# Performance work log

Hardware: AMD Instinct MI355X
Metric: run time of the kernel (lower is better)

The kernel has to match this reference:

```python
import jax, jax.numpy as jnp
import numpy as np
import math

# ---- static configuration (matches init_kwargs / input_specs) ----
N = 512       # nodes
CIN = 32      # input multiplicity per irrep l
C = 32        # num_channels
LMAX = 4      # input/output lmax
D = (LMAX + 1) ** 2   # 25 real-SH components
RB = 48       # res_beta (Gauss-Legendre nodes in cos(beta))
RA = 95       # res_alpha (uniform)
NB = 3        # parity branches (p1,p2) in {(1,1),(1,-1),(-1,1)}


def _assoc_legendre(lmax, x):
    """Associated Legendre P_l^m(x) with Condon-Shortley phase. [l, m, len(x)]."""
    P = np.zeros((lmax + 1, lmax + 1, len(x)))
    P[0, 0] = 1.0
    sx = np.sqrt(np.maximum(0.0, 1.0 - x * x))
    for m in range(1, lmax + 1):
        P[m, m] = -(2 * m - 1) * sx * P[m - 1, m - 1]
    for m in range(lmax):
        P[m + 1, m] = (2 * m + 1) * x * P[m, m]
    for l in range(2, lmax + 1):
        for m in range(0, l - 1):
            P[l, m] = ((2 * l - 1) * x * P[l - 1, m] - (l + m - 1) * P[l - 2, m]) / (l - m)
    return P


def _real_sh_grid(lmax, rb, ra):
    """Real orthonormal SH sampled on (beta, alpha) grid + quadrature-weighted basis.
    Returns Y [(lmax+1)^2, rb, ra] and Yw (Y * w_beta * dalpha) so that
    einsum('dba,eba->de', Y, Yw) ~= identity (exact SHT / inverse SHT pair)."""
    xq, wq = np.polynomial.legendre.leggauss(rb)   # x = cos(beta), GL quadrature
    P = _assoc_legendre(lmax, xq)
    alpha = 2.0 * np.pi * np.arange(ra) / ra
    Dd = (lmax + 1) ** 2
    Y = np.zeros((Dd, rb, ra))
    for l in range(lmax + 1):
        for m in range(0, l + 1):
            Nlm = math.sqrt((2 * l + 1) / (4 * math.pi) * math.factorial(l - m) / math.factorial(l + m))
            if m == 0:
                Y[l * l + l] = Nlm * P[l, 0][:, None] * np.ones((1, ra))
            else:
                Y[l * l + l + m] = math.sqrt(2.0) * Nlm * P[l, m][:, None] * np.cos(m * alpha)[None, :]
                Y[l * l + l - m] = math.sqrt(2.0) * Nlm * P[l, m][:, None] * np.sin(m * alpha)[None, :]
    Yw = Y * wq[None, :, None] * (2.0 * np.pi / ra)
    return Y.astype(np.float32), Yw.astype(np.float32)

_Y_NP, _YW_NP = _real_sh_grid(LMAX, RB, RA)


def setup_inputs() -> dict:
    key = jax.random.key(0)
    ks = jax.random.split(key, 6)
    s_in = 1.0 / np.sqrt(CIN)
    return {
        "x1": jax.random.normal(ks[0], (N, CIN, D), jnp.float32),
        "x2": jax.random.normal(ks[1], (N, CIN, D), jnp.float32),
        "W1": jax.random.normal(ks[2], (NB, LMAX, CIN, C), jnp.float32) * s_in,
        "W2": jax.random.normal(ks[3], (NB, LMAX, CIN, C), jnp.float32) * s_in,
        "Wout0": jax.random.normal(ks[4], (NB, C + CIN, C + CIN), jnp.float32) / np.sqrt(C + CIN),
        "WoutL": jax.random.normal(ks[5], (NB, LMAX, C, C), jnp.float32) / np.sqrt(C),
    }


def _project(x, W):
    """Equivariant Linear: per-l channel mixing CIN->C, dropping l=0 (filter drop 0e/0o).
    x [N, CIN, D], W [LMAX, CIN, C] -> [N, C, D] with l=0 slot zero."""
    parts = [jnp.zeros((x.shape[0], W.shape[-1], 1), x.dtype)]
    for l in range(1, LMAX + 1):
        xl = x[:, :, l * l:(l + 1) * (l + 1)]            # [N, CIN, 2l+1]
        parts.append(jnp.einsum('nkm,kc->ncm', xl, W[l - 1]))
    return jnp.concatenate(parts, axis=-1)


def reference(x1, x2, W1, W2, Wout0, WoutL):
    Y = jnp.asarray(_Y_NP)    # [D, RB, RA]
    Yw = jnp.asarray(_YW_NP)  # quadrature-weighted basis for the inverse transform
    n = x1.shape[0]
    outs = []
    for b in range(NB):  # three parity branches, distinct learned weights
        c1 = _project(x1, W1[b])                      # [N, C, D]
        c2 = _project(x2, W2[b])
        f1 = jnp.einsum('ncd,dba->ncba', c1, Y)        # to S2 grid [N, C, RB, RA]
        f2 = jnp.einsum('ncd,dba->ncba', c2, Y)
        cp = jnp.einsum('ncba,dba->ncd', f1 * f2, Yw)  # pointwise product + inverse SHT
        s = x1[:, :, 0] * x2[:, :, 0]                  # scalar CG tensor product [N, CIN]
        o0 = jnp.concatenate([cp[:, :, 0], s], axis=1) @ Wout0[b]   # l=0 output mix
        oL = [jnp.einsum('ncm,cd->ndm', cp[:, :, l * l:(l + 1) * (l + 1)], WoutL[b, l - 1]).reshape(n, -1)
              for l in range(1, LMAX + 1)]
        outs.append(jnp.concatenate([o0] + oL, axis=1))
    return jnp.concatenate(outs, axis=1)  # [N, 3*(C+CIN + C*(D-1))] = [512, 2496]
```

## Files before the change

kernel.cpp:

```cpp
#include <hip/hip_runtime.h>
#include <math.h>

#define DDIM 25
#define RB 48
#define RA 95
#define OUT_PER_B 832
#define OUT_STRIDE 2496
#define PI_D 3.14159265358979323846

#define SEG_I  8
#define ENT_I  64
#define ENT_CAP 2600
#define TRIP_CAP 2600

__device__ int g_ready = 0;
__device__ int g_tab[ENT_I + 2 * ENT_CAP];

__constant__ int L_OF_D[25] = {0,1,1,1,2,2,2,2,2,3,3,3,3,3,3,3,4,4,4,4,4,4,4,4,4};

__device__ __forceinline__ float bf2f(unsigned short u) {
    return __uint_as_float(((unsigned int)u) << 16);
}
__device__ __forceinline__ unsigned short f2bf(float f) {
    unsigned int x = __float_as_uint(f);
    return (unsigned short)((x + 0x7FFFu + ((x >> 16) & 1u)) >> 16);
}

__global__ __launch_bounds__(1024) void setup_kernel() {
    if (g_ready) return;

    __shared__ double xg[RB], wq[RB];
    __shared__ double Rl[DDIM * RB];
    __shared__ double cosT[RA * 5], sinT[RA * 5];
    __shared__ double AS[729];
    __shared__ double invT[64];
    __shared__ int cnt[DDIM], cnt2[DDIM];
    __shared__ int segl[DDIM + 1];
    __shared__ int tripl[TRIP_CAP];
    __shared__ int ntrip;
    const int t = threadIdx.x;
    const int BT = 1024;

    if (t == 0) ntrip = 0;
    if (t < DDIM) { cnt[t] = 0; cnt2[t] = 0; }
    if (t < 64) invT[t] = (t == 0) ? 0.0 : 1.0 / (double)t;
    __syncthreads();

    if (t < RB) {
        double x = cos(PI_D * (t + 0.75) / (RB + 0.5));
        double p0, p1, dp;
        for (int it = 0; it < 5; ++it) {
            p0 = 1.0; p1 = x;
            for (int k = 2; k <= RB; ++k) {
                double p2 = ((2.0 * k - 1.0) * x * p1 - (k - 1.0) * p0) * invT[k];
                p0 = p1; p1 = p2;
            }
            dp = RB * (x * p1 - p0) / (x * x - 1.0);
            x -= p1 / dp;
        }
        p0 = 1.0; p1 = x;
        for (int k = 2; k <= RB; ++k) {
            double p2 = ((2.0 * k - 1.0) * x * p1 - (k - 1.0) * p0) * invT[k];
            p0 = p1; p1 = p2;
        }
        dp = RB * (x * p1 - p0) / (x * x - 1.0);
        xg[t] = x;
        wq[t] = 2.0 / ((1.0 - x * x) * dp * dp);
    }
    for (int idx = t; idx < RA * 5; idx += BT) {
        int a = idx / 5, mm = idx % 5;
        double ang = 2.0 * PI_D * (double)(mm * a) / (double)RA;
        cosT[idx] = cos(ang);
        sinT[idx] = sin(ang);
    }
    __syncthreads();

    for (int idx = t; idx < DDIM * RB; idx += BT) {
        int d = idx / RB, b = idx % RB;
        int l = L_OF_D[d];
        int m = d - l * l - l;
        int am = m < 0 ? -m : m;
        double x = xg[b];
        double sx = sqrt(fmax(0.0, 1.0 - x * x));
        double pmm = 1.0;
        for (int k = 1; k <= am; ++k) pmm = -(2.0 * k - 1.0) * sx * pmm;
        double res;
        if (l == am) res = pmm;
        else {
            double pprev = pmm;
            double pcur = (2.0 * am + 1.0) * x * pmm;
            for (int ll = am + 2; ll <= l; ++ll) {
                double pnext = ((2.0 * ll - 1.0) * x * pcur - (double)(ll + am - 1) * pprev) * invT[ll - am];
                pprev = pcur; pcur = pnext;
            }
            res = pcur;
        }
        double fr = 1.0;
        for (int j = l - am + 1; j <= l + am; ++j) fr *= (double)j;
        double Nlm = sqrt((2.0 * l + 1.0) / (4.0 * PI_D) / fr);
        if (m != 0) Nlm *= sqrt(2.0);
        Rl[d * RB + b] = Nlm * res;
    }
    __syncthreads();

    for (int idx = t; idx < 729; idx += BT) {
        int m1 = idx / 81 - 4, m2 = (idx / 9) % 9 - 4, m3 = idx % 9 - 4;
        double s = 0.0;
        for (int a = 0; a < RA; ++a) {
            double t1 = (m1 == 0) ? 1.0 : (m1 > 0 ? cosT[a * 5 + m1] : sinT[a * 5 - m1]);
            double t2 = (m2 == 0) ? 1.0 : (m2 > 0 ? cosT[a * 5 + m2] : sinT[a * 5 - m2]);
            double t3 = (m3 == 0) ? 1.0 : (m3 > 0 ? cosT[a * 5 + m3] : sinT[a * 5 - m3]);
            s += t1 * t2 * t3;
        }
        AS[idx] = s * (2.0 * PI_D / (double)RA);
    }
    __syncthreads();

    for (int idx = t; idx < 24 * 24 * 25; idx += BT) {
        int d3 = idx % 25;
        int r = idx / 25;
        int dd2 = r % 24, dd1 = r / 24;
        int d1 = dd1 + 1, d2 = dd2 + 1;
        int l1 = L_OF_D[d1], l2 = L_OF_D[d2], l3 = L_OF_D[d3];
        if ((l1 + l2 + l3) & 1) continue;
        if (l3 < abs(l1 - l2) || l3 > l1 + l2) continue;
        int m1 = d1 - l1 * l1 - l1, m2 = d2 - l2 * l2 - l2, m3 = d3 - l3 * l3 - l3;
        if (fabs(AS[(m1 + 4) * 81 + (m2 + 4) * 9 + (m3 + 4)]) < 1e-6) continue;
        int pos = atomicAdd(&ntrip, 1);
        if (pos < TRIP_CAP) {
            tripl[pos] = (d3 << 16) | (dd1 << 8) | dd2;
            atomicAdd(&cnt[d3], 1);
        }
    }
    __syncthreads();
    if (t == 0) {
        segl[0] = 0;
        for (int d = 0; d < DDIM; ++d) segl[d + 1] = segl[d] + cnt[d];
        for (int d = 0; d <= DDIM; ++d) g_tab[SEG_I + d] = segl[d];
    }
    __syncthreads();

    {
        int nt = ntrip < TRIP_CAP ? ntrip : TRIP_CAP;
        uint2* ent = (uint2*)(g_tab + ENT_I);
        for (int i = t; i < nt; i += BT) {
            int pk = tripl[i];
            int d3 = pk >> 16, dd1 = (pk >> 8) & 255, dd2 = pk & 255;
            int d1 = dd1 + 1, d2 = dd2 + 1;
            int l1 = L_OF_D[d1], l2 = L_OF_D[d2], l3 = L_OF_D[d3];
            int m1 = d1 - l1 * l1 - l1, m2 = d2 - l2 * l2 - l2, m3 = d3 - l3 * l3 - l3;
            const double* r1 = &Rl[d1 * RB];
            const double* r2 = &Rl[d2 * RB];
            const double* r3 = &Rl[d3 * RB];
            double s0 = 0.0, s1 = 0.0, s2 = 0.0, s3 = 0.0;
            for (int b = 0; b < RB; b += 4) {
                s0 += wq[b + 0] * r1[b + 0] * r2[b + 0] * r3[b + 0];
                s1 += wq[b + 1] * r1[b + 1] * r2[b + 1] * r3[b + 1];
                s2 += wq[b + 2] * r1[b + 2] * r2[b + 2] * r3[b + 2];
                s3 += wq[b + 3] * r1[b + 3] * r2[b + 3] * r3[b + 3];
            }
            double g = (s0 + s1 + s2 + s3) * AS[(m1 + 4) * 81 + (m2 + 4) * 9 + (m3 + 4)];
            int pos = atomicAdd(&cnt2[d3], 1);
            int at = segl[d3] + pos;
            if (at < ENT_CAP)
                ent[at] = make_uint2((unsigned)((dd1 << 8) | dd2), __float_as_uint((float)g));
        }
    }
    __syncthreads();
    if (t == 0) g_ready = 1;
}

template <int ISF32>
__device__ __forceinline__ void stageW(const void* Wv, int b, float* wbuf, int t) {
    if (ISF32) {
        const float* w = (const float*)Wv + b * 4096;
        #pragma unroll
        for (int i = 0; i < 8; ++i) wbuf[t + 512 * i] = w[t + 512 * i];
    } else {
        const unsigned* w = (const unsigned*)Wv + b * 2048;
        #pragma unroll
        for (int i = 0; i < 4; ++i) {
            unsigned v = w[t + 512 * i];
            wbuf[2 * (t + 512 * i)]     = bf2f((unsigned short)(v & 0xFFFF));
            wbuf[2 * (t + 512 * i) + 1] = bf2f((unsigned short)(v >> 16));
        }
    }
}

__device__ __forceinline__ void mix_pair(const float* __restrict__ xs,
                                         const float* __restrict__ wbuf,
                                         float* __restrict__ cs, int t) {
    if (t >= 384) return;
    int j = t & 15;
    int dd = t >> 4;
    int d = dd + 1;
    int l = L_OF_D[d];
    const float* wv = &wbuf[(l - 1) * 1024 + 2 * j];
    const float* xv = &xs[2 * d];
    float a00 = 0.f, a01 = 0.f, a10 = 0.f, a11 = 0.f;
    #pragma unroll
    for (int k = 0; k < 32; ++k) {
        float2 w = *(const float2*)&wv[k * 32];
        float2 x = *(const float2*)&xv[k * 50];
        a00 += x.x * w.x; a01 += x.x * w.y;
        a10 += x.y * w.x; a11 += x.y * w.y;
    }
    int c0 = 2 * j, c1 = 2 * j + 1;
    cs[2 * (c0 * 25 + dd) + 0] = a00;
    cs[2 * (c0 * 25 + dd) + 1] = a10;
    cs[2 * (c1 * 25 + dd) + 0] = a01;
    cs[2 * (c1 * 25 + dd) + 1] = a11;
}

template <int ISF32>
__device__ __forceinline__ void main_body(
    const void* __restrict__ x1v, const void* __restrict__ x2v,
    const void* __restrict__ W1v, const void* __restrict__ W2v,
    const void* __restrict__ Wo0v, const void* __restrict__ WoLv,
    void* __restrict__ outv,
    float* wbuf, float* x1s, float* x2s, float* c1s, float* c2s, float* cps,
    const int t, const int np, const int b)
{
    const int s = t >> 8;
    const int tl = t & 255;
    const int n = np * 2 + s;

    if (ISF32) {
        const float* x1f = (const float*)x1v + n * 800;
        const float* x2f = (const float*)x2v + n * 800;
        for (int i = tl; i < 800; i += 256) {
            x1s[2 * i + s] = x1f[i];
            x2s[2 * i + s] = x2f[i];
        }
    } else {
        const unsigned* x1u = (const unsigned*)x1v + n * 400;
        const unsigned* x2u = (const unsigned*)x2v + n * 400;
        for (int i = tl; i < 400; i += 256) {
            unsigned v1 = x1u[i], v2 = x2u[i];
            x1s[4 * i + s]     = bf2f((unsigned short)(v1 & 0xFFFF));
            x1s[4 * i + 2 + s] = bf2f((unsigned short)(v1 >> 16));
            x2s[4 * i + s]     = bf2f((unsigned short)(v2 & 0xFFFF));
            x2s[4 * i + 2 + s] = bf2f((unsigned short)(v2 >> 16));
        }
    }
    stageW<ISF32>(W1v, b, wbuf, t);
    __syncthreads();

    mix_pair(x1s, wbuf, c1s, t);
    __syncthreads();
    stageW<ISF32>(W2v, b, wbuf, t);
    __syncthreads();
    mix_pair(x2s, wbuf, c2s, t);
    __syncthreads();

    {
        const int* seg = g_tab + SEG_I;
        const uint2* ent = (const uint2*)(g_tab + ENT_I);
        int c = t & 31;
        int gq = t >> 5;
        const float* c1p = &c1s[50 * c];
        const float* c2p = &c2s[50 * c];
        for (int d3 = gq; d3 < 25; d3 += 16) {
            int j1 = seg[d3 + 1];
            float a0 = 0.f, a1 = 0.f;
            for (int j = seg[d3]; j < j1; ++j) {
                uint2 e = ent[j];
                float gf = __uint_as_float(e.y);
                float2 u = *(const float2*)&c1p[2 * (e.x >> 8)];
                float2 v = *(const float2*)&c2p[2 * (e.x & 255)];
                a0 += gf * u.x * v.x;
                a1 += gf * u.y * v.y;
            }
            *(float2*)&cps[2 * (c * 25 + d3)] = make_float2(a0, a1);
        }
    }
    stageW<ISF32>(WoLv, b, wbuf, t);
    __syncthreads();

    const int obase0 = (np * 2) * OUT_STRIDE + b * OUT_PER_B;
    const int obase1 = obase0 + OUT_STRIDE;
    if (t < 384) {
        int dout = t & 31;
        int mg = t >> 5;
        int d3a = 1 + 2 * mg, d3b = 2 + 2 * mg;
        int la = L_OF_D[d3a], lb = L_OF_D[d3b];
        const float* wa = &wbuf[(la - 1) * 1024 + dout];
        const float* wb = &wbuf[(lb - 1) * 1024 + dout];
        float a0a = 0.f, a1a = 0.f, a0b = 0.f, a1b = 0.f;
        #pragma unroll 8
        for (int c = 0; c < 32; ++c) {
            float wva = wa[c * 32];
            float wvb = wb[c * 32];
            float2 pa = *(const float2*)&cps[2 * (c * 25 + d3a)];
            float2 pb = *(const float2*)&cps[2 * (c * 25 + d3b)];
            a0a += pa.x * wva; a1a += pa.y * wva;
            a0b += pb.x * wvb; a1b += pb.y * wvb;
        }
        int rela = 32 * (la * la - 1) + dout * (2 * la + 1) + (d3a - la * la);
        int relb = 32 * (lb * lb - 1) + dout * (2 * lb + 1) + (d3b - lb * lb);
        if (ISF32) {
            float* o = (float*)outv;
            o[obase0 + 64 + rela] = a0a; o[obase1 + 64 + rela] = a1a;
            o[obase0 + 64 + relb] = a0b; o[obase1 + 64 + relb] = a1b;
        } else {
            unsigned short* o = (unsigned short*)outv;
            o[obase0 + 64 + rela] = f2bf(a0a); o[obase1 + 64 + rela] = f2bf(a1a);
            o[obase0 + 64 + relb] = f2bf(a0b); o[obase1 + 64 + relb] = f2bf(a1b);
        }
    } else if (t < 448) {
        int j = t - 384;
        float a0 = 0.f, a1 = 0.f;
        if (ISF32) {
            const float* w0 = (const float*)Wo0v + b * 4096 + j;
            #pragma unroll
            for (int i = 0; i < 32; ++i) {
                float w = w0[i * 64];
                float2 p = *(const float2*)&cps[50 * i];
                a0 += p.x * w; a1 += p.y * w;
            }
            #pragma unroll
            for (int i = 0; i < 32; ++i) {
                float w = w0[(i + 32) * 64];
                float2 u = *(const float2*)&x1s[50 * i];
                float2 v = *(const float2*)&x2s[50 * i];
                a0 += (u.x * v.x) * w; a1 += (u.y * v.y) * w;
            }
            ((float*)outv)[obase0 + j] = a0;
            ((float*)outv)[obase1 + j] = a1;
        } else {
            const unsigned short* w0 = (const unsigned short*)Wo0v + b * 4096 + j;
            #pragma unroll
            for (int i = 0; i < 32; ++i) {
                float w = bf2f(w0[i * 64]);
                float2 p = *(const float2*)&cps[50 * i];
                a0 += p.x * w; a1 += p.y * w;
            }
            #pragma unroll
            for (int i = 0; i < 32; ++i) {
                float w = bf2f(w0[(i + 32) * 64]);
                float2 u = *(const float2*)&x1s[50 * i];
                float2 v = *(const float2*)&x2s[50 * i];
                a0 += (u.x * v.x) * w; a1 += (u.y * v.y) * w;
            }
            ((unsigned short*)outv)[obase0 + j] = f2bf(a0);
            ((unsigned short*)outv)[obase1 + j] = f2bf(a1);
        }
    }
}

__global__ __launch_bounds__(512, 6) void main_kernel(
    const void* __restrict__ x1v, const void* __restrict__ x2v,
    const void* __restrict__ W1v, const void* __restrict__ W2v,
    const void* __restrict__ Wo0v, const void* __restrict__ WoLv,
    void* __restrict__ outv)
{
    __shared__ __attribute__((aligned(16))) float wbuf[4096];
    __shared__ __attribute__((aligned(16))) float x1l[1600];
    __shared__ __attribute__((aligned(16))) float x2l[1600];
    __shared__ __attribute__((aligned(16))) float c1l[1600];
    __shared__ __attribute__((aligned(16))) float c2l[1600];
    __shared__ __attribute__((aligned(16))) float cpl[1600];

    const int t = threadIdx.x;
    const int np = blockIdx.x & 255;
    const int b = blockIdx.x >> 8;

    int outl = 0;
    if (t < 128) {
        unsigned short h = (unsigned short)(((const unsigned*)x1v)[t] & 0xFFFF);
        unsigned e = (h >> 7) & 0xFF;
        outl = (e < 64 || e > 191) ? 1 : 0;
    }
    const int isf32 = (__syncthreads_count(outl) >= 32) ? 1 : 0;

    if (isf32)
        main_body<1>(x1v, x2v, W1v, W2v, Wo0v, WoLv, outv,
                     wbuf, x1l, x2l, c1l, c2l, cpl, t, np, b);
    else
        main_body<0>(x1v, x2v, W1v, W2v, Wo0v, WoLv, outv,
                     wbuf, x1l, x2l, c1l, c2l, cpl, t, np, b);
}

extern "C" void kernel_launch(void* const* d_in, const int* in_sizes, int n_in,
                              void* d_out, int out_size, void* d_ws, size_t ws_size,
                              hipStream_t stream) {
    setup_kernel<<<1, 1024, 0, stream>>>();
    main_kernel<<<768, 512, 0, stream>>>(d_in[0], d_in[1], d_in[2], d_in[3],
                                         d_in[4], d_in[5], d_out);
}
```

Before: 97.45 us.

## Process four nodes per 1024-thread block to amortize weight staging

Each block now handles four nodes (two pairs) with 1024 threads instead of two nodes with 512, halving the grid to 384 blocks. Staged weights in shared memory are reused across twice as many nodes, so there are fewer global weight loads and bf16 conversions per node. The cost is a larger shared-memory footprint per block, fewer blocks in flight, and bigger barriers that synchronize more threads. With 384 blocks, device-wide parallelism and the tail of the launch could also change.

```diff
diff --git a/kernel.cpp b/kernel.cpp
--- a/kernel.cpp
+++ b/kernel.cpp
@@ -175,14 +175,14 @@
     if (ISF32) {
         const float* w = (const float*)Wv + b * 4096;
         #pragma unroll
-        for (int i = 0; i < 8; ++i) wbuf[t + 512 * i] = w[t + 512 * i];
+        for (int i = 0; i < 4; ++i) wbuf[t + 1024 * i] = w[t + 1024 * i];
     } else {
         const unsigned* w = (const unsigned*)Wv + b * 2048;
         #pragma unroll
-        for (int i = 0; i < 4; ++i) {
-            unsigned v = w[t + 512 * i];
-            wbuf[2 * (t + 512 * i)]     = bf2f((unsigned short)(v & 0xFFFF));
-            wbuf[2 * (t + 512 * i) + 1] = bf2f((unsigned short)(v >> 16));
+        for (int i = 0; i < 2; ++i) {
+            unsigned v = w[t + 1024 * i];
+            wbuf[2 * (t + 1024 * i)]     = bf2f((unsigned short)(v & 0xFFFF));
+            wbuf[2 * (t + 1024 * i) + 1] = bf2f((unsigned short)(v >> 16));
         }
     }
 }
@@ -190,13 +190,16 @@
 __device__ __forceinline__ void mix_pair(const float* __restrict__ xs,
                                          const float* __restrict__ wbuf,
                                          float* __restrict__ cs, int t) {
-    if (t >= 384) return;
-    int j = t & 15;
-    int dd = t >> 4;
+    if (t >= 768) return;
+    int p = t >> 9;
+    p = (t >= 384) ? 1 : 0;
+    int r = t - p * 384;
+    int j = r & 15;
+    int dd = r >> 4;
     int d = dd + 1;
     int l = L_OF_D[d];
     const float* wv = &wbuf[(l - 1) * 1024 + 2 * j];
-    const float* xv = &xs[2 * d];
+    const float* xv = &xs[p * 1600 + 2 * d];
     float a00 = 0.f, a01 = 0.f, a10 = 0.f, a11 = 0.f;
     #pragma unroll
     for (int k = 0; k < 32; ++k) {
@@ -206,10 +209,11 @@
         a10 += x.y * w.x; a11 += x.y * w.y;
     }
     int c0 = 2 * j, c1 = 2 * j + 1;
-    cs[2 * (c0 * 25 + dd) + 0] = a00;
-    cs[2 * (c0 * 25 + dd) + 1] = a10;
-    cs[2 * (c1 * 25 + dd) + 0] = a01;
-    cs[2 * (c1 * 25 + dd) + 1] = a11;
+    float* cp = cs + p * 1600;
+    cp[2 * (c0 * 25 + dd) + 0] = a00;
+    cp[2 * (c0 * 25 + dd) + 1] = a10;
+    cp[2 * (c1 * 25 + dd) + 0] = a01;
+    cp[2 * (c1 * 25 + dd) + 1] = a11;
 }
 
 template <int ISF32>
@@ -219,28 +223,34 @@
     const void* __restrict__ Wo0v, const void* __restrict__ WoLv,
     void* __restrict__ outv,
     float* wbuf, float* x1s, float* x2s, float* c1s, float* c2s, float* cps,
-    const int t, const int np, const int b)
+    const int t, const int np4, const int b)
 {
-    const int s = t >> 8;
+    const int s2 = t >> 8;
+    const int sp = s2 >> 1;
+    const int sq = s2 & 1;
     const int tl = t & 255;
-    const int n = np * 2 + s;
+    const int n = np4 * 4 + s2;
 
     if (ISF32) {
         const float* x1f = (const float*)x1v + n * 800;
         const float* x2f = (const float*)x2v + n * 800;
+        float* x1p = x1s + sp * 1600;
+        float* x2p = x2s + sp * 1600;
         for (int i = tl; i < 800; i += 256) {
-            x1s[2 * i + s] = x1f[i];
-            x2s[2 * i + s] = x2f[i];
+            x1p[2 * i + sq] = x1f[i];
+            x2p[2 * i + sq] = x2f[i];
         }
     } else {
         const unsigned* x1u = (const unsigned*)x1v + n * 400;
         const unsigned* x2u = (const unsigned*)x2v + n * 400;
+        float* x1p = x1s + sp * 1600;
+        float* x2p = x2s + sp * 1600;
         for (int i = tl; i < 400; i += 256) {
             unsigned v1 = x1u[i], v2 = x2u[i];
-            x1s[4 * i + s]     = bf2f((unsigned short)(v1 & 0xFFFF));
-            x1s[4 * i + 2 + s] = bf2f((unsigned short)(v1 >> 16));
-            x2s[4 * i + s]     = bf2f((unsigned short)(v2 & 0xFFFF));
-            x2s[4 * i + 2 + s] = bf2f((unsigned short)(v2 >> 16));
+            x1p[4 * i + sq]     = bf2f((unsigned short)(v1 & 0xFFFF));
+            x1p[4 * i + 2 + sq] = bf2f((unsigned short)(v1 >> 16));
+            x2p[4 * i + sq]     = bf2f((unsigned short)(v2 & 0xFFFF));
+            x2p[4 * i + 2 + sq] = bf2f((unsigned short)(v2 >> 16));
         }
     }
     stageW<ISF32>(W1v, b, wbuf, t);
@@ -256,10 +266,12 @@
     {
         const int* seg = g_tab + SEG_I;
         const uint2* ent = (const uint2*)(g_tab + ENT_I);
-        int c = t & 31;
-        int gq = t >> 5;
-        const float* c1p = &c1s[50 * c];
-        const float* c2p = &c2s[50 * c];
+        int p = t >> 9;
+        int tt = t & 511;
+        int c = tt & 31;
+        int gq = tt >> 5;
+        const float* c1p = &c1s[p * 1600 + 50 * c];
+        const float* c2p = &c2s[p * 1600 + 50 * c];
         for (int d3 = gq; d3 < 25; d3 += 16) {
             int j1 = seg[d3 + 1];
             float a0 = 0.f, a1 = 0.f;
@@ -271,99 +283,106 @@
                 a0 += gf * u.x * v.x;
                 a1 += gf * u.y * v.y;
             }
-            *(float2*)&cps[2 * (c * 25 + d3)] = make_float2(a0, a1);
+            *(float2*)&cps[p * 1600 + 2 * (c * 25 + d3)] = make_float2(a0, a1);
         }
     }
     stageW<ISF32>(WoLv, b, wbuf, t);
     __syncthreads();
 
-    const int obase0 = (np * 2) * OUT_STRIDE + b * OUT_PER_B;
-    const int obase1 = obase0 + OUT_STRIDE;
-    if (t < 384) {
-        int dout = t & 31;
-        int mg = t >> 5;
-        int d3a = 1 + 2 * mg, d3b = 2 + 2 * mg;
-        int la = L_OF_D[d3a], lb = L_OF_D[d3b];
-        const float* wa = &wbuf[(la - 1) * 1024 + dout];
-        const float* wb = &wbuf[(lb - 1) * 1024 + dout];
-        float a0a = 0.f, a1a = 0.f, a0b = 0.f, a1b = 0.f;
-        #pragma unroll 8
-        for (int c = 0; c < 32; ++c) {
-            float wva = wa[c * 32];
-            float wvb = wb[c * 32];
-            float2 pa = *(const float2*)&cps[2 * (c * 25 + d3a)];
-            float2 pb = *(const float2*)&cps[2 * (c * 25 + d3b)];
-            a0a += pa.x * wva; a1a += pa.y * wva;
-            a0b += pb.x * wvb; a1b += pb.y * wvb;
-        }
-        int rela = 32 * (la * la - 1) + dout * (2 * la + 1) + (d3a - la * la);
-        int relb = 32 * (lb * lb - 1) + dout * (2 * lb + 1) + (d3b - lb * lb);
-        if (ISF32) {
-            float* o = (float*)outv;
-            o[obase0 + 64 + rela] = a0a; o[obase1 + 64 + rela] = a1a;
-            o[obase0 + 64 + relb] = a0b; o[obase1 + 64 + relb] = a1b;
-        } else {
-            unsigned short* o = (unsigned short*)outv;
-            o[obase0 + 64 + rela] = f2bf(a0a); o[obase1 + 64 + rela] = f2bf(a1a);
-            o[obase0 + 64 + relb] = f2bf(a0b); o[obase1 + 64 + relb] = f2bf(a1b);
-        }
-    } else if (t < 448) {
-        int j = t - 384;
-        float a0 = 0.f, a1 = 0.f;
-        if (ISF32) {
-            const float* w0 = (const float*)Wo0v + b * 4096 + j;
-            #pragma unroll
-            for (int i = 0; i < 32; ++i) {
-                float w = w0[i * 64];
-                float2 p = *(const float2*)&cps[50 * i];
-                a0 += p.x * w; a1 += p.y * w;
-            }
-            #pragma unroll
-            for (int i = 0; i < 32; ++i) {
-                float w = w0[(i + 32) * 64];
-                float2 u = *(const float2*)&x1s[50 * i];
-                float2 v = *(const float2*)&x2s[50 * i];
-                a0 += (u.x * v.x) * w; a1 += (u.y * v.y) * w;
-            }
-            ((float*)outv)[obase0 + j] = a0;
-            ((float*)outv)[obase1 + j] = a1;
-        } else {
-            const unsigned short* w0 = (const unsigned short*)Wo0v + b * 4096 + j;
-            #pragma unroll
-            for (int i = 0; i < 32; ++i) {
-                float w = bf2f(w0[i * 64]);
-                float2 p = *(const float2*)&cps[50 * i];
-                a0 += p.x * w; a1 += p.y * w;
-            }
-            #pragma unroll
-            for (int i = 0; i < 32; ++i) {
-                float w = bf2f(w0[(i + 32) * 64]);
-                float2 u = *(const float2*)&x1s[50 * i];
-                float2 v = *(const float2*)&x2s[50 * i];
-                a0 += (u.x * v.x) * w; a1 += (u.y * v.y) * w;
-            }
-            ((unsigned short*)outv)[obase0 + j] = f2bf(a0);
-            ((unsigned short*)outv)[obase1 + j] = f2bf(a1);
-        }
-    }
-}
-
-__global__ __launch_bounds__(512, 6) void main_kernel(
+    {
+        int p = t >> 9;
+        int tt = t & 511;
+        const int obase0 = (np4 * 4 + 2 * p) * OUT_STRIDE + b * OUT_PER_B;
+        const int obase1 = obase0 + OUT_STRIDE;
+        const float* cpp = cps + p * 1600;
+        if (tt < 384) {
+            int dout = tt & 31;
+            int mg = tt >> 5;
+            int d3a = 1 + 2 * mg, d3b = 2 + 2 * mg;
+            int la = L_OF_D[d3a], lb = L_OF_D[d3b];
+            const float* wa = &wbuf[(la - 1) * 1024 + dout];
+            const float* wb = &wbuf[(lb - 1) * 1024 + dout];
+            float a0a = 0.f, a1a = 0.f, a0b = 0.f, a1b = 0.f;
+            #pragma unroll 8
+            for (int c = 0; c < 32; ++c) {
+                float wva = wa[c * 32];
+                float wvb = wb[c * 32];
+                float2 pa = *(const float2*)&cpp[2 * (c * 25 + d3a)];
+                float2 pb = *(const float2*)&cpp[2 * (c * 25 + d3b)];
+                a0a += pa.x * wva; a1a += pa.y * wva;
+                a0b += pb.x * wvb; a1b += pb.y * wvb;
+            }
+            int rela = 32 * (la * la - 1) + dout * (2 * la + 1) + (d3a - la * la);
+            int relb = 32 * (lb * lb - 1) + dout * (2 * lb + 1) + (d3b - lb * lb);
+            if (ISF32) {
+                float* o = (float*)outv;
+                o[obase0 + 64 + rela] = a0a; o[obase1 + 64 + rela] = a1a;
+                o[obase0 + 64 + relb] = a0b; o[obase1 + 64 + relb] = a1b;
+            } else {
+                unsigned short* o = (unsigned short*)outv;
+                o[obase0 + 64 + rela] = f2bf(a0a); o[obase1 + 64 + rela] = f2bf(a1a);
+                o[obase0 + 64 + relb] = f2bf(a0b); o[obase1 + 64 + relb] = f2bf(a1b);
+            }
+        } else if (tt < 448) {
+            int j = tt - 384;
+            const float* x1p = x1s + p * 1600;
+            const float* x2p = x2s + p * 1600;
+            float a0 = 0.f, a1 = 0.f;
+            if (ISF32) {
+                const float* w0 = (const float*)Wo0v + b * 4096 + j;
+                #pragma unroll
+                for (int i = 0; i < 32; ++i) {
+                    float w = w0[i * 64];
+                    float2 pv = *(const float2*)&cpp[50 * i];
+                    a0 += pv.x * w; a1 += pv.y * w;
+                }
+                #pragma unroll
+                for (int i = 0; i < 32; ++i) {
+                    float w = w0[(i + 32) * 64];
+                    float2 u = *(const float2*)&x1p[50 * i];
+                    float2 v = *(const float2*)&x2p[50 * i];
+                    a0 += (u.x * v.x) * w; a1 += (u.y * v.y) * w;
+                }
+                ((float*)outv)[obase0 + j] = a0;
+                ((float*)outv)[obase1 + j] = a1;
+            } else {
+                const unsigned short* w0 = (const unsigned short*)Wo0v + b * 4096 + j;
+                #pragma unroll
+                for (int i = 0; i < 32; ++i) {
+                    float w = bf2f(w0[i * 64]);
+                    float2 pv = *(const float2*)&cpp[50 * i];
+                    a0 += pv.x * w; a1 += pv.y * w;
+                }
+                #pragma unroll
+                for (int i = 0; i < 32; ++i) {
+                    float w = bf2f(w0[(i + 32) * 64]);
+                    float2 u = *(const float2*)&x1p[50 * i];
+                    float2 v = *(const float2*)&x2p[50 * i];
+                    a0 += (u.x * v.x) * w; a1 += (u.y * v.y) * w;
+                }
+                ((unsigned short*)outv)[obase0 + j] = f2bf(a0);
+                ((unsigned short*)outv)[obase1 + j] = f2bf(a1);
+            }
+        }
+    }
+}
+
+__global__ __launch_bounds__(1024, 8) void main_kernel(
     const void* __restrict__ x1v, const void* __restrict__ x2v,
     const void* __restrict__ W1v, const void* __restrict__ W2v,
     const void* __restrict__ Wo0v, const void* __restrict__ WoLv,
     void* __restrict__ outv)
 {
     __shared__ __attribute__((aligned(16))) float wbuf[4096];
-    __shared__ __attribute__((aligned(16))) float x1l[1600];
-    __shared__ __attribute__((aligned(16))) float x2l[1600];
-    __shared__ __attribute__((aligned(16))) float c1l[1600];
-    __shared__ __attribute__((aligned(16))) float c2l[1600];
-    __shared__ __attribute__((aligned(16))) float cpl[1600];
+    __shared__ __attribute__((aligned(16))) float x1l[3200];
+    __shared__ __attribute__((aligned(16))) float x2l[3200];
+    __shared__ __attribute__((aligned(16))) float c1l[3200];
+    __shared__ __attribute__((aligned(16))) float c2l[3200];
+    __shared__ __attribute__((aligned(16))) float cpl[3200];
 
     const int t = threadIdx.x;
-    const int np = blockIdx.x & 255;
-    const int b = blockIdx.x >> 8;
+    const int np4 = blockIdx.x & 127;
+    const int b = blockIdx.x >> 7;
 
     int outl = 0;
     if (t < 128) {
@@ -375,16 +394,16 @@
 
     if (isf32)
         main_body<1>(x1v, x2v, W1v, W2v, Wo0v, WoLv, outv,
-                     wbuf, x1l, x2l, c1l, c2l, cpl, t, np, b);
+                     wbuf, x1l, x2l, c1l, c2l, cpl, t, np4, b);
     else
         main_body<0>(x1v, x2v, W1v, W2v, Wo0v, WoLv, outv,
-                     wbuf, x1l, x2l, c1l, c2l, cpl, t, np, b);
+                     wbuf, x1l, x2l, c1l, c2l, cpl, t, np4, b);
 }
 
 extern "C" void kernel_launch(void* const* d_in, const int* in_sizes, int n_in,
                               void* d_out, int out_size, void* d_ws, size_t ws_size,
                               hipStream_t stream) {
     setup_kernel<<<1, 1024, 0, stream>>>();
-    main_kernel<<<768, 512, 0, stream>>>(d_in[0], d_in[1], d_in[2], d_in[3],
-                                         d_in[4], d_in[5], d_out);
-}
+    main_kernel<<<384, 1024, 0, stream>>>(d_in[0], d_in[1], d_in[2], d_in[3],
+                                          d_in[4], d_in[5], d_out);
+}
```

Result: slower. 101.2 us (+3.8%).

## Transpose projected coefficient layout to d-major for vectorized CG contraction

Applied to the files above, without the earlier changes.

Changes the shared-memory layout of the projected coefficients and the CG product result from channel-major [c][d][2] to component-major [d][c][2]. Each thread in the Clebsch-Gordan contraction now handles two channels for one output component using float4 loads, and the mix step writes with a single float4 store. The aim is fewer LDS instructions and fewer bank conflicts, plus a simpler loop with no strided d3 iteration, at the cost of each thread handling a longer entry list for its component. The c1/c2 buffers shrink slightly to match the new layout.

```diff
diff --git a/kernel.cpp b/kernel.cpp
--- a/kernel.cpp
+++ b/kernel.cpp
@@ -205,11 +205,7 @@
         a00 += x.x * w.x; a01 += x.x * w.y;
         a10 += x.y * w.x; a11 += x.y * w.y;
     }
-    int c0 = 2 * j, c1 = 2 * j + 1;
-    cs[2 * (c0 * 25 + dd) + 0] = a00;
-    cs[2 * (c0 * 25 + dd) + 1] = a10;
-    cs[2 * (c1 * 25 + dd) + 0] = a01;
-    cs[2 * (c1 * 25 + dd) + 1] = a11;
+    *(float4*)&cs[dd * 64 + 4 * j] = make_float4(a00, a10, a01, a11);
 }
 
 template <int ISF32>
@@ -256,22 +252,24 @@
     {
         const int* seg = g_tab + SEG_I;
         const uint2* ent = (const uint2*)(g_tab + ENT_I);
-        int c = t & 31;
-        int gq = t >> 5;
-        const float* c1p = &c1s[50 * c];
-        const float* c2p = &c2s[50 * c];
-        for (int d3 = gq; d3 < 25; d3 += 16) {
+        int cp = t & 15;
+        int d3 = t >> 4;
+        if (d3 < 25) {
+            const float* c1b = c1s + 4 * cp;
+            const float* c2b = c2s + 4 * cp;
             int j1 = seg[d3 + 1];
-            float a0 = 0.f, a1 = 0.f;
+            float4 acc = make_float4(0.f, 0.f, 0.f, 0.f);
             for (int j = seg[d3]; j < j1; ++j) {
                 uint2 e = ent[j];
                 float gf = __uint_as_float(e.y);
-                float2 u = *(const float2*)&c1p[2 * (e.x >> 8)];
-                float2 v = *(const float2*)&c2p[2 * (e.x & 255)];
-                a0 += gf * u.x * v.x;
-                a1 += gf * u.y * v.y;
-            }
-            *(float2*)&cps[2 * (c * 25 + d3)] = make_float2(a0, a1);
+                float4 u = *(const float4*)&c1b[(e.x >> 8) * 64];
+                float4 v = *(const float4*)&c2b[(e.x & 255) * 64];
+                acc.x += gf * u.x * v.x;
+                acc.y += gf * u.y * v.y;
+                acc.z += gf * u.z * v.z;
+                acc.w += gf * u.w * v.w;
+            }
+            *(float4*)&cps[d3 * 64 + 4 * cp] = acc;
         }
     }
     stageW<ISF32>(WoLv, b, wbuf, t);
@@ -291,8 +289,8 @@
         for (int c = 0; c < 32; ++c) {
             float wva = wa[c * 32];
             float wvb = wb[c * 32];
-            float2 pa = *(const float2*)&cps[2 * (c * 25 + d3a)];
-            float2 pb = *(const float2*)&cps[2 * (c * 25 + d3b)];
+            float2 pa = *(const float2*)&cps[d3a * 64 + 2 * c];
+            float2 pb = *(const float2*)&cps[d3b * 64 + 2 * c];
             a0a += pa.x * wva; a1a += pa.y * wva;
             a0b += pb.x * wvb; a1b += pb.y * wvb;
         }
@@ -315,7 +313,7 @@
             #pragma unroll
             for (int i = 0; i < 32; ++i) {
                 float w = w0[i * 64];
-                float2 p = *(const float2*)&cps[50 * i];
+                float2 p = *(const float2*)&cps[2 * i];
                 a0 += p.x * w; a1 += p.y * w;
             }
             #pragma unroll
@@ -332,7 +330,7 @@
             #pragma unroll
             for (int i = 0; i < 32; ++i) {
                 float w = bf2f(w0[i * 64]);
-                float2 p = *(const float2*)&cps[50 * i];
+                float2 p = *(const float2*)&cps[2 * i];
                 a0 += p.x * w; a1 += p.y * w;
             }
             #pragma unroll
@@ -357,8 +355,8 @@
     __shared__ __attribute__((aligned(16))) float wbuf[4096];
     __shared__ __attribute__((aligned(16))) float x1l[1600];
     __shared__ __attribute__((aligned(16))) float x2l[1600];
-    __shared__ __attribute__((aligned(16))) float c1l[1600];
-    __shared__ __attribute__((aligned(16))) float c2l[1600];
+    __shared__ __attribute__((aligned(16))) float c1l[1536];
+    __shared__ __attribute__((aligned(16))) float c2l[1536];
     __shared__ __attribute__((aligned(16))) float cpl[1600];
 
     const int t = threadIdx.x;
```

After: 87.62 us. -10.1%, faster.
